# Kernel optimization log

Measured on AMD Instinct MI355X. Metric: run time of the kernel, lower is better.

Reference implementation:

```python
import jax, jax.numpy as jnp
import numpy as np

N_NODES = 50000
N_EDGES = 640000
IN_C, HID_C, OUT_C = 64, 128, 64


def _glorot(key, fan_in, fan_out):
    lim = float(np.sqrt(6.0 / (fan_in + fan_out)))
    return jax.random.uniform(key, (fan_in, fan_out), jnp.float32, -lim, lim)


def setup_inputs() -> dict:
    key = jax.random.key(0)
    ks = jax.random.split(key, 16)
    x = jax.random.normal(ks[0], (N_NODES, IN_C), jnp.float32)
    edge_index = jax.random.randint(ks[1], (2, N_EDGES), 0, N_NODES, jnp.int64)
    # SAGEConv params: out = mean_aggr(x_j) @ Wl + x @ Wr + b
    dims = [(IN_C, HID_C), (HID_C, HID_C), (HID_C, OUT_C)]
    params = {}
    for i, (fi, fo) in enumerate(dims):
        params[f"Wl{i}"] = _glorot(ks[2 + 3 * i], fi, fo)
        params[f"Wr{i}"] = _glorot(ks[3 + 3 * i], fi, fo)
        params[f"b{i}"] = jnp.zeros((fo,), jnp.float32)
    # classifier: Linear(64,32) -> ReLU -> Linear(32,1) -> Sigmoid (dropout off in eval)
    params["Wc1"] = _glorot(ks[11], OUT_C, 32)
    params["bc1"] = jnp.zeros((32,), jnp.float32)
    params["Wc2"] = _glorot(ks[12], 32, 1)
    params["bc2"] = jnp.zeros((1,), jnp.float32)
    return {"x": x, "edge_index": edge_index, **params}


def _sage_conv(x, src, dst, Wl, Wr, b):
    # gather neighbor (source) features along edges, mean-aggregate at target
    msgs = x[src]                                                    # [E, C]
    agg = jax.ops.segment_sum(msgs, dst, num_segments=N_NODES)      # [N, C]
    deg = jax.ops.segment_sum(jnp.ones((src.shape[0], 1), x.dtype), dst,
                              num_segments=N_NODES)                 # [N, 1]
    agg = agg / jnp.maximum(deg, 1.0)
    return agg @ Wl + x @ Wr + b


def reference(x, edge_index, Wl0, Wr0, b0, Wl1, Wr1, b1, Wl2, Wr2, b2,
              Wc1, bc1, Wc2, bc2):
    src, dst = edge_index[0], edge_index[1]
    h = jax.nn.relu(_sage_conv(x, src, dst, Wl0, Wr0, b0))
    h = jax.nn.relu(_sage_conv(h, src, dst, Wl1, Wr1, b1))
    h = _sage_conv(h, src, dst, Wl2, Wr2, b2)                       # [N, 64]
    h = jax.nn.relu(h @ Wc1 + bc1)                                  # [N, 32]
    return jax.nn.sigmoid(h @ Wc2 + bc2)                            # [N, 1]
```

## Files before the change

kernel.cpp:

```cpp
#include <hip/hip_runtime.h>
#include <math.h>

#define NN 50000
#define NE 640000
#define CAP 64
#define TM 64

typedef short short8 __attribute__((ext_vector_type(8)));
typedef float f32x4  __attribute__((ext_vector_type(4)));

__device__ __forceinline__ unsigned bfr(float f) {
    unsigned u = __float_as_uint(f);
    return (u + 0x7FFFu + ((u >> 16) & 1u)) >> 16;
}
__device__ __forceinline__ unsigned pk2(float a, float b) { return bfr(a) | (bfr(b) << 16); }
__device__ __forceinline__ float bflo(unsigned u) { return __uint_as_float(u << 16); }
__device__ __forceinline__ float bfhi(unsigned u) { return __uint_as_float(u & 0xFFFF0000u); }

__device__ __forceinline__ void packOne(const float* Wl, const float* Wr,
                                        unsigned short* wp, int idx,
                                        int CIN, int COUT) {
    int k = idx / COUT, n = idx % COUT;
    float v = (k < CIN) ? Wl[k * COUT + n] : Wr[(k - CIN) * COUT + n];
    int kt = k >> 5, quad = (k >> 3) & 3, j = k & 7;
    int nt = n >> 4, l16 = n & 15;
    int NT = COUT / 16;
    wp[(((kt * NT + nt) * 64) + quad * 16 + l16) * 8 + j] = (unsigned short)bfr(v);
}

template <int CIN, int COUT, bool RELU, bool CLS>
__device__ __forceinline__ void
fused_layer(const unsigned* __restrict__ Fu, const unsigned short* __restrict__ Fs,
            const int* __restrict__ nbr, const int* __restrict__ cnt,
            const unsigned short* __restrict__ Wpack, const float* __restrict__ bias,
            unsigned short* __restrict__ outp,
            const unsigned short* __restrict__ WpackC, const float* __restrict__ bc1,
            const float* __restrict__ Wc2, const float* __restrict__ bc2,
            float* __restrict__ outf,
            short* __restrict__ lds, int tile, int t) {
    constexpr int RU = CIN / 2;
    constexpr int PC = RU / 16;
    constexpr int RS = CIN + 8;
    constexpr int RSu = RS / 2;
    constexpr int KT = (2 * CIN) / 32;
    constexpr int NT = COUT / 16;
    constexpr int CS = 136;

    const int g = t >> 4, lg = t & 15;
    const int wave = t >> 6, lane = t & 63;
    const int quad = lane >> 4, l16 = lane & 15;

#pragma unroll 1
    for (int i = 0; i < TM / 16; ++i) {
        const int rloc = g * (TM / 16) + i;
        const int gw = tile * TM + rloc;
        unsigned* lrow = (unsigned*)lds + rloc * RSu + lg * PC;
        if (gw < NN) {
            const int deg = cnt[gw];
            const int m = (deg < CAP) ? deg : CAP;
            float a[2 * PC] = {};
            for (int base = 0; base < m; base += 16) {
                int idx = NN;
                if (base + lg < m) idx = nbr[gw * CAP + base + lg];
                if (PC == 2) {
                    uint2 u[16];
#pragma unroll
                    for (int j = 0; j < 16; ++j) {
                        const int n = __shfl(idx, j, 16);
                        u[j] = *(const uint2*)(Fu + (size_t)n * RU + lg * 2);
                    }
#pragma unroll
                    for (int j = 0; j < 16; ++j) {
                        a[0] += bflo(u[j].x); a[1] += bfhi(u[j].x);
                        a[2] += bflo(u[j].y); a[3] += bfhi(u[j].y);
                    }
                } else {
                    uint4 u[16];
#pragma unroll
                    for (int j = 0; j < 16; ++j) {
                        const int n = __shfl(idx, j, 16);
                        u[j] = *(const uint4*)(Fu + (size_t)n * RU + lg * 4);
                    }
#pragma unroll
                    for (int j = 0; j < 16; ++j) {
                        a[0] += bflo(u[j].x); a[1] += bfhi(u[j].x);
                        a[2] += bflo(u[j].y); a[3] += bfhi(u[j].y);
                        a[4] += bflo(u[j].z); a[5] += bfhi(u[j].z);
                        a[6] += bflo(u[j].w); a[7] += bfhi(u[j].w);
                    }
                }
            }
            const float di = 1.0f / (float)((deg > 1) ? deg : 1);
            if (PC == 2)
                *(uint2*)lrow = make_uint2(pk2(a[0] * di, a[1] * di),
                                           pk2(a[2] * di, a[3] * di));
            else
                *(uint4*)lrow = make_uint4(pk2(a[0] * di, a[1] * di),
                                           pk2(a[2] * di, a[3] * di),
                                           pk2(a[4] * di, a[5] * di),
                                           pk2(a[6] * di, a[7] * di));
        } else {
            if (PC == 2) *(uint2*)lrow = make_uint2(0u, 0u);
            else         *(uint4*)lrow = make_uint4(0u, 0u, 0u, 0u);
        }
    }
    __syncthreads();

    const int rbase = tile * TM + wave * 16;
    int r0 = rbase + l16; if (r0 >= NN) r0 = NN - 1;
    const int rl0 = wave * 16 + l16;

    f32x4 acc[NT] = {};
#pragma unroll
    for (int kt = 0; kt < KT; ++kt) {
        short8 a0;
        if (kt < KT / 2)
            a0 = *(const short8*)(lds + rl0 * RS + kt * 32 + quad * 8);
        else
            a0 = *(const short8*)(Fs + (size_t)r0 * CIN + (kt * 32 - CIN) + quad * 8);
#pragma unroll
        for (int nt = 0; nt < NT; ++nt) {
            const short8 bfrag = *(const short8*)(Wpack + (size_t)((kt * NT + nt) * 64 + lane) * 8);
            acc[nt] = __builtin_amdgcn_mfma_f32_16x16x32_bf16(a0, bfrag, acc[nt], 0, 0, 0);
        }
    }
    __syncthreads();

    if constexpr (!CLS) {
#pragma unroll
        for (int nt = 0; nt < NT; ++nt) {
            const float bb = bias[nt * 16 + l16];
#pragma unroll
            for (int rg = 0; rg < 4; ++rg) {
                const int rloc = wave * 16 + quad * 4 + rg;
                float v = acc[nt][rg] + bb;
                if (RELU) v = fmaxf(v, 0.f);
                lds[rloc * CS + nt * 16 + l16] = (short)(unsigned short)bfr(v);
            }
        }
        __syncthreads();
        constexpr int CH = COUT / 8;
        for (int idx = t; idx < TM * CH; idx += 256) {
            const int row = idx / CH, c8 = idx % CH;
            const int gr = tile * TM + row;
            if (gr < NN)
                *(uint4*)(outp + (size_t)gr * COUT + c8 * 8) =
                    *(const uint4*)(lds + row * CS + c8 * 8);
        }
    } else {
        constexpr int HS = 72;
#pragma unroll
        for (int nt = 0; nt < NT; ++nt) {
            const float bb = bias[nt * 16 + l16];
#pragma unroll
            for (int rg = 0; rg < 4; ++rg) {
                const int rloc = wave * 16 + quad * 4 + rg;
                lds[rloc * HS + nt * 16 + l16] =
                    (short)(unsigned short)bfr(acc[nt][rg] + bb);
            }
        }
        __syncthreads();

        f32x4 sacc[2] = {};
        const int rloc = wave * 16 + l16;
#pragma unroll
        for (int kt2 = 0; kt2 < 2; ++kt2) {
            const short8 af = *(const short8*)(lds + rloc * HS + kt2 * 32 + quad * 8);
#pragma unroll
            for (int nt2 = 0; nt2 < 2; ++nt2) {
                const short8 bf = *(const short8*)(WpackC + (size_t)((kt2 * 2 + nt2) * 64 + lane) * 8);
                sacc[nt2] = __builtin_amdgcn_mfma_f32_16x16x32_bf16(af, bf, sacc[nt2], 0, 0, 0);
            }
        }

        const float b1a = bc1[l16], b1b = bc1[16 + l16];
        const float w2a = Wc2[l16], w2b = Wc2[16 + l16];
        const float b2v = bc2[0];
#pragma unroll
        for (int rg = 0; rg < 4; ++rg) {
            float p = fmaxf(sacc[0][rg] + b1a, 0.f) * w2a +
                      fmaxf(sacc[1][rg] + b1b, 0.f) * w2b;
#pragma unroll
            for (int off = 1; off < 16; off <<= 1) p += __shfl_xor(p, off);
            if (l16 == 0) {
                const int row = tile * TM + wave * 16 + quad * 4 + rg;
                if (row < NN) outf[row] = 1.0f / (1.0f + expf(-(p + b2v)));
            }
        }
    }
}

template <int CIN, int COUT, bool RELU, bool CLS>
__global__ __launch_bounds__(256) void
k_fused(const unsigned* __restrict__ Fu, const unsigned short* __restrict__ Fs,
        const int* __restrict__ nbr, const int* __restrict__ cnt,
        const unsigned short* __restrict__ Wpack, const float* __restrict__ bias,
        unsigned short* __restrict__ outp,
        const unsigned short* __restrict__ WpackC, const float* __restrict__ bc1,
        const float* __restrict__ Wc2, const float* __restrict__ bc2,
        float* __restrict__ outf) {
    __shared__ __align__(16) short lds[TM * 136];
    fused_layer<CIN, COUT, RELU, CLS>(Fu, Fs, nbr, cnt, Wpack, bias, outp,
                                      WpackC, bc1, Wc2, bc2, outf,
                                      lds, blockIdx.x, threadIdx.x);
}

__global__ __launch_bounds__(256) void
k_prep(const int* __restrict__ src, const int* __restrict__ dst,
       int* __restrict__ cnt, int* __restrict__ nbr,
       const float* __restrict__ x, unsigned* __restrict__ xb,
       const float* Wl0, const float* Wr0, const float* Wl1, const float* Wr1,
       const float* Wl2, const float* Wr2, const float* Wc1,
       unsigned short* wp0, unsigned short* wp1, unsigned short* wp2,
       unsigned short* wpc, unsigned short* h0b, unsigned short* h1b) {
    const int b = blockIdx.x, t = threadIdx.x;
    if (b < 2500) {
        int e = b * 256 + t;
        if (e < NE) {
            int d = dst[e];
            int p = atomicAdd(&cnt[d], 1);
            if (p < CAP) nbr[d * CAP + p] = src[e];
        }
        if (b == 0) {
            if (t < 32) xb[(size_t)NN * 32 + t] = 0u;
            else if (t < 96) ((unsigned*)h0b)[(size_t)NN * 64 + (t - 32)] = 0u;
            else if (t < 160) ((unsigned*)h1b)[(size_t)NN * 64 + (t - 96)] = 0u;
        }
    } else if (b < 5625) {
        int i = (b - 2500) * 256 + t;
        if (i < NN * 16) {
            float4 v = ((const float4*)x)[i];
            ((uint2*)xb)[i] = make_uint2(pk2(v.x, v.y), pk2(v.z, v.w));
        }
    } else {
        int idx = (b - 5625) * 256 + t;
        if (idx < 16384) packOne(Wl0, Wr0, wp0, idx, 64, 128);
        else if (idx < 49152) packOne(Wl1, Wr1, wp1, idx - 16384, 128, 128);
        else if (idx < 65536) packOne(Wl2, Wr2, wp2, idx - 49152, 128, 64);
        else if (idx < 67584) packOne(Wc1, Wc1, wpc, idx - 65536, 64, 32);
    }
}

extern "C" void kernel_launch(void* const* d_in, const int* in_sizes, int n_in,
                              void* d_out, int out_size, void* d_ws, size_t ws_size,
                              hipStream_t stream) {
    const float* x   = (const float*)d_in[0];
    const int*   ei  = (const int*)d_in[1];
    const int*   src = ei;
    const int*   dst = ei + NE;
    const float* Wl0 = (const float*)d_in[2];
    const float* Wr0 = (const float*)d_in[3];
    const float* b0  = (const float*)d_in[4];
    const float* Wl1 = (const float*)d_in[5];
    const float* Wr1 = (const float*)d_in[6];
    const float* b1  = (const float*)d_in[7];
    const float* Wl2 = (const float*)d_in[8];
    const float* Wr2 = (const float*)d_in[9];
    const float* b2  = (const float*)d_in[10];
    const float* Wc1 = (const float*)d_in[11];
    const float* bc1 = (const float*)d_in[12];
    const float* Wc2 = (const float*)d_in[13];
    const float* bc2 = (const float*)d_in[14];
    float* out = (float*)d_out;

    char*  ws   = (char*)d_ws;
    int*   cnt  = (int*)(ws);
    unsigned short* wp0 = (unsigned short*)(ws + (size_t)256 * 1024);
    unsigned short* wp1 = (unsigned short*)(ws + (size_t)352 * 1024);
    unsigned short* wp2 = (unsigned short*)(ws + (size_t)448 * 1024);
    unsigned short* wpc = (unsigned short*)(ws + (size_t)512 * 1024);
    int*   nbr  = (int*)(ws + (size_t)1 * (1 << 20));
    unsigned short* xb   = (unsigned short*)(ws + (size_t)16 * (1 << 20));
    unsigned short* h0b  = (unsigned short*)(ws + (size_t)40 * (1 << 20));
    unsigned short* h1b  = (unsigned short*)(ws + (size_t)56 * (1 << 20));

    hipMemsetAsync(cnt, 0, (size_t)NN * sizeof(int), stream);

    const int B = 256;
    const int NTILE = (NN + TM - 1) / TM;

    k_prep<<<5889, B, 0, stream>>>(src, dst, cnt, nbr, x, (unsigned*)xb,
                                   Wl0, Wr0, Wl1, Wr1, Wl2, Wr2, Wc1,
                                   wp0, wp1, wp2, wpc, h0b, h1b);

    k_fused<64, 128, true, false><<<NTILE, B, 0, stream>>>(
        (const unsigned*)xb, xb, nbr, cnt, wp0, b0, h0b,
        nullptr, nullptr, nullptr, nullptr, nullptr);

    k_fused<128, 128, true, false><<<NTILE, B, 0, stream>>>(
        (const unsigned*)h0b, h0b, nbr, cnt, wp1, b1, h1b,
        nullptr, nullptr, nullptr, nullptr, nullptr);

    k_fused<128, 64, false, true><<<NTILE, B, 0, stream>>>(
        (const unsigned*)h1b, h1b, nbr, cnt, wp2, b2, nullptr,
        wpc, bc1, Wc2, bc2, out);
}
```

Baseline: 216.9 us.

## Halve row tile, prefetch neighbor indices early, restrict MFMA to active waves

The row tile per block drops from 64 to 32, so there are twice as many blocks for the 50k nodes and each 16-lane group aggregates 2 rows instead of 4. Both rows' degrees and first neighbor-index chunks are loaded up front so their latency overlaps, and later index loads are issued at the end of each gather iteration. Only the first two waves now run the MFMA GEMM and classifier; the other waves wait at matching barriers. The aim is more parallelism and better hiding of latency in the memory-bound gather, at the cost of idle waves during the compute phase and more weight-fragment reloads across blocks.

```diff
diff --git a/kernel.cpp b/kernel.cpp
--- a/kernel.cpp
+++ b/kernel.cpp
@@ -4,7 +4,7 @@
 #define NN 50000
 #define NE 640000
 #define CAP 64
-#define TM 64
+#define TM 32
 
 typedef short short8 __attribute__((ext_vector_type(8)));
 typedef float f32x4  __attribute__((ext_vector_type(4)));
@@ -50,95 +50,130 @@
     const int wave = t >> 6, lane = t & 63;
     const int quad = lane >> 4, l16 = lane & 15;
 
+    {
+        const int gw0 = tile * TM + g * 2;
+        const int gw1 = gw0 + 1;
+        int deg0 = 0, deg1 = 0;
+        if (gw0 < NN) deg0 = cnt[gw0];
+        if (gw1 < NN) deg1 = cnt[gw1];
+        const int m0 = (deg0 < CAP) ? deg0 : CAP;
+        const int m1 = (deg1 < CAP) ? deg1 : CAP;
+        int idx0 = NN, idx1 = NN;
+        if (lg < m0) idx0 = nbr[gw0 * CAP + lg];
+        if (lg < m1) idx1 = nbr[gw1 * CAP + lg];
+
 #pragma unroll 1
-    for (int i = 0; i < TM / 16; ++i) {
-        const int rloc = g * (TM / 16) + i;
-        const int gw = tile * TM + rloc;
-        unsigned* lrow = (unsigned*)lds + rloc * RSu + lg * PC;
-        if (gw < NN) {
-            const int deg = cnt[gw];
-            const int m = (deg < CAP) ? deg : CAP;
-            float a[2 * PC] = {};
-            for (int base = 0; base < m; base += 16) {
-                int idx = NN;
-                if (base + lg < m) idx = nbr[gw * CAP + base + lg];
-                if (PC == 2) {
-                    uint2 u[16];
-#pragma unroll
-                    for (int j = 0; j < 16; ++j) {
-                        const int n = __shfl(idx, j, 16);
-                        u[j] = *(const uint2*)(Fu + (size_t)n * RU + lg * 2);
+        for (int rr = 0; rr < 2; ++rr) {
+            const int gw = rr ? gw1 : gw0;
+            const int m  = rr ? m1  : m0;
+            const int deg = rr ? deg1 : deg0;
+            int idx = rr ? idx1 : idx0;
+            const int rloc = g * 2 + rr;
+            unsigned* lrow = (unsigned*)lds + rloc * RSu + lg * PC;
+            if (gw < NN) {
+                float a[2 * PC] = {};
+                for (int base = 0; ; ) {
+                    if (PC == 2) {
+                        uint2 u[16];
+#pragma unroll
+                        for (int j = 0; j < 16; ++j) {
+                            const int n = __shfl(idx, j, 16);
+                            u[j] = *(const uint2*)(Fu + (size_t)n * RU + lg * 2);
+                        }
+#pragma unroll
+                        for (int j = 0; j < 16; ++j) {
+                            a[0] += bflo(u[j].x); a[1] += bfhi(u[j].x);
+                            a[2] += bflo(u[j].y); a[3] += bfhi(u[j].y);
+                        }
+                    } else {
+                        uint4 u[16];
+#pragma unroll
+                        for (int j = 0; j < 16; ++j) {
+                            const int n = __shfl(idx, j, 16);
+                            u[j] = *(const uint4*)(Fu + (size_t)n * RU + lg * 4);
+                        }
+#pragma unroll
+                        for (int j = 0; j < 16; ++j) {
+                            a[0] += bflo(u[j].x); a[1] += bfhi(u[j].x);
+                            a[2] += bflo(u[j].y); a[3] += bfhi(u[j].y);
+                            a[4] += bflo(u[j].z); a[5] += bfhi(u[j].z);
+                            a[6] += bflo(u[j].w); a[7] += bfhi(u[j].w);
+                        }
                     }
-#pragma unroll
-                    for (int j = 0; j < 16; ++j) {
-                        a[0] += bflo(u[j].x); a[1] += bfhi(u[j].x);
-                        a[2] += bflo(u[j].y); a[3] += bfhi(u[j].y);
-                    }
-                } else {
-                    uint4 u[16];
-#pragma unroll
-                    for (int j = 0; j < 16; ++j) {
-                        const int n = __shfl(idx, j, 16);
-                        u[j] = *(const uint4*)(Fu + (size_t)n * RU + lg * 4);
-                    }
-#pragma unroll
-                    for (int j = 0; j < 16; ++j) {
-                        a[0] += bflo(u[j].x); a[1] += bfhi(u[j].x);
-                        a[2] += bflo(u[j].y); a[3] += bfhi(u[j].y);
-                        a[4] += bflo(u[j].z); a[5] += bfhi(u[j].z);
-                        a[6] += bflo(u[j].w); a[7] += bfhi(u[j].w);
-                    }
-                }
-            }
-            const float di = 1.0f / (float)((deg > 1) ? deg : 1);
-            if (PC == 2)
-                *(uint2*)lrow = make_uint2(pk2(a[0] * di, a[1] * di),
-                                           pk2(a[2] * di, a[3] * di));
-            else
-                *(uint4*)lrow = make_uint4(pk2(a[0] * di, a[1] * di),
-                                           pk2(a[2] * di, a[3] * di),
-                                           pk2(a[4] * di, a[5] * di),
-                                           pk2(a[6] * di, a[7] * di));
-        } else {
-            if (PC == 2) *(uint2*)lrow = make_uint2(0u, 0u);
-            else         *(uint4*)lrow = make_uint4(0u, 0u, 0u, 0u);
+                    base += 16;
+                    if (base >= m) break;
+                    idx = NN;
+                    if (base + lg < m) idx = nbr[gw * CAP + base + lg];
+                }
+                const float di = 1.0f / (float)((deg > 1) ? deg : 1);
+                if (PC == 2)
+                    *(uint2*)lrow = make_uint2(pk2(a[0] * di, a[1] * di),
+                                               pk2(a[2] * di, a[3] * di));
+                else
+                    *(uint4*)lrow = make_uint4(pk2(a[0] * di, a[1] * di),
+                                               pk2(a[2] * di, a[3] * di),
+                                               pk2(a[4] * di, a[5] * di),
+                                               pk2(a[6] * di, a[7] * di));
+            } else {
+                if (PC == 2) *(uint2*)lrow = make_uint2(0u, 0u);
+                else         *(uint4*)lrow = make_uint4(0u, 0u, 0u, 0u);
+            }
         }
     }
     __syncthreads();
 
-    const int rbase = tile * TM + wave * 16;
-    int r0 = rbase + l16; if (r0 >= NN) r0 = NN - 1;
-    const int rl0 = wave * 16 + l16;
-
-    f32x4 acc[NT] = {};
-#pragma unroll
-    for (int kt = 0; kt < KT; ++kt) {
-        short8 a0;
-        if (kt < KT / 2)
-            a0 = *(const short8*)(lds + rl0 * RS + kt * 32 + quad * 8);
-        else
-            a0 = *(const short8*)(Fs + (size_t)r0 * CIN + (kt * 32 - CIN) + quad * 8);
-#pragma unroll
-        for (int nt = 0; nt < NT; ++nt) {
-            const short8 bfrag = *(const short8*)(Wpack + (size_t)((kt * NT + nt) * 64 + lane) * 8);
-            acc[nt] = __builtin_amdgcn_mfma_f32_16x16x32_bf16(a0, bfrag, acc[nt], 0, 0, 0);
-        }
+    if (wave < TM / 16) {
+        const int rbase = tile * TM + wave * 16;
+        int r0 = rbase + l16; if (r0 >= NN) r0 = NN - 1;
+        const int rl0 = wave * 16 + l16;
+
+        f32x4 acc[NT] = {};
+#pragma unroll
+        for (int kt = 0; kt < KT; ++kt) {
+            short8 a0;
+            if (kt < KT / 2)
+                a0 = *(const short8*)(lds + rl0 * RS + kt * 32 + quad * 8);
+            else
+                a0 = *(const short8*)(Fs + (size_t)r0 * CIN + (kt * 32 - CIN) + quad * 8);
+#pragma unroll
+            for (int nt = 0; nt < NT; ++nt) {
+                const short8 bfrag = *(const short8*)(Wpack + (size_t)((kt * NT + nt) * 64 + lane) * 8);
+                acc[nt] = __builtin_amdgcn_mfma_f32_16x16x32_bf16(a0, bfrag, acc[nt], 0, 0, 0);
+            }
+        }
+        __syncthreads();
+
+        if constexpr (!CLS) {
+#pragma unroll
+            for (int nt = 0; nt < NT; ++nt) {
+                const float bb = bias[nt * 16 + l16];
+#pragma unroll
+                for (int rg = 0; rg < 4; ++rg) {
+                    const int rloc = wave * 16 + quad * 4 + rg;
+                    float v = acc[nt][rg] + bb;
+                    if (RELU) v = fmaxf(v, 0.f);
+                    lds[rloc * CS + nt * 16 + l16] = (short)(unsigned short)bfr(v);
+                }
+            }
+        } else {
+            constexpr int HS = 72;
+#pragma unroll
+            for (int nt = 0; nt < NT; ++nt) {
+                const float bb = bias[nt * 16 + l16];
+#pragma unroll
+                for (int rg = 0; rg < 4; ++rg) {
+                    const int rloc = wave * 16 + quad * 4 + rg;
+                    lds[rloc * HS + nt * 16 + l16] =
+                        (short)(unsigned short)bfr(acc[nt][rg] + bb);
+                }
+            }
+        }
+    } else {
+        __syncthreads();
     }
     __syncthreads();
 
     if constexpr (!CLS) {
-#pragma unroll
-        for (int nt = 0; nt < NT; ++nt) {
-            const float bb = bias[nt * 16 + l16];
-#pragma unroll
-            for (int rg = 0; rg < 4; ++rg) {
-                const int rloc = wave * 16 + quad * 4 + rg;
-                float v = acc[nt][rg] + bb;
-                if (RELU) v = fmaxf(v, 0.f);
-                lds[rloc * CS + nt * 16 + l16] = (short)(unsigned short)bfr(v);
-            }
-        }
-        __syncthreads();
         constexpr int CH = COUT / 8;
         for (int idx = t; idx < TM * CH; idx += 256) {
             const int row = idx / CH, c8 = idx % CH;
@@ -148,43 +183,33 @@
                     *(const uint4*)(lds + row * CS + c8 * 8);
         }
     } else {
-        constexpr int HS = 72;
-#pragma unroll
-        for (int nt = 0; nt < NT; ++nt) {
-            const float bb = bias[nt * 16 + l16];
+        if (wave < TM / 16) {
+            constexpr int HS = 72;
+            f32x4 sacc[2] = {};
+            const int rloc = wave * 16 + l16;
+#pragma unroll
+            for (int kt2 = 0; kt2 < 2; ++kt2) {
+                const short8 af = *(const short8*)(lds + rloc * HS + kt2 * 32 + quad * 8);
+#pragma unroll
+                for (int nt2 = 0; nt2 < 2; ++nt2) {
+                    const short8 bf = *(const short8*)(WpackC + (size_t)((kt2 * 2 + nt2) * 64 + lane) * 8);
+                    sacc[nt2] = __builtin_amdgcn_mfma_f32_16x16x32_bf16(af, bf, sacc[nt2], 0, 0, 0);
+                }
+            }
+
+            const float b1a = bc1[l16], b1b = bc1[16 + l16];
+            const float w2a = Wc2[l16], w2b = Wc2[16 + l16];
+            const float b2v = bc2[0];
 #pragma unroll
             for (int rg = 0; rg < 4; ++rg) {
-                const int rloc = wave * 16 + quad * 4 + rg;
-                lds[rloc * HS + nt * 16 + l16] =
-                    (short)(unsigned short)bfr(acc[nt][rg] + bb);
-            }
-        }
-        __syncthreads();
-
-        f32x4 sacc[2] = {};
-        const int rloc = wave * 16 + l16;
-#pragma unroll
-        for (int kt2 = 0; kt2 < 2; ++kt2) {
-            const short8 af = *(const short8*)(lds + rloc * HS + kt2 * 32 + quad * 8);
-#pragma unroll
-            for (int nt2 = 0; nt2 < 2; ++nt2) {
-                const short8 bf = *(const short8*)(WpackC + (size_t)((kt2 * 2 + nt2) * 64 + lane) * 8);
-                sacc[nt2] = __builtin_amdgcn_mfma_f32_16x16x32_bf16(af, bf, sacc[nt2], 0, 0, 0);
-            }
-        }
-
-        const float b1a = bc1[l16], b1b = bc1[16 + l16];
-        const float w2a = Wc2[l16], w2b = Wc2[16 + l16];
-        const float b2v = bc2[0];
-#pragma unroll
-        for (int rg = 0; rg < 4; ++rg) {
-            float p = fmaxf(sacc[0][rg] + b1a, 0.f) * w2a +
-                      fmaxf(sacc[1][rg] + b1b, 0.f) * w2b;
-#pragma unroll
-            for (int off = 1; off < 16; off <<= 1) p += __shfl_xor(p, off);
-            if (l16 == 0) {
-                const int row = tile * TM + wave * 16 + quad * 4 + rg;
-                if (row < NN) outf[row] = 1.0f / (1.0f + expf(-(p + b2v)));
+                float p = fmaxf(sacc[0][rg] + b1a, 0.f) * w2a +
+                          fmaxf(sacc[1][rg] + b1b, 0.f) * w2b;
+#pragma unroll
+                for (int off = 1; off < 16; off <<= 1) p += __shfl_xor(p, off);
+                if (l16 == 0) {
+                    const int row = tile * TM + wave * 16 + quad * 4 + rg;
+                    if (row < NN) outf[row] = 1.0f / (1.0f + expf(-(p + b2v)));
+                }
             }
         }
     }
```

New measurement: 221.2 us. No clear change (+2.0%).
